# Kernel tuning notes

Hardware: AMD Instinct MI355X
Metric: run time of the kernel (lower is better)

Reference implementation:

```python
import jax, jax.numpy as jnp
import numpy as np

WINDOW = (2, 7, 7)
SHIFT = (1, 3, 3)
HEADS = 4


def _rel_pos_index(ws):
    coords = np.stack(np.meshgrid(*[np.arange(w) for w in ws], indexing='ij'))  # (3, wd, wh, ww)
    cf = coords.reshape(3, -1)
    rel = cf[:, :, None] - cf[:, None, :]  # (3, N, N)
    rel = rel.transpose(1, 2, 0).astype(np.int64)
    rel[:, :, 0] += ws[0] - 1
    rel[:, :, 1] += ws[1] - 1
    rel[:, :, 2] += ws[2] - 1
    rel[:, :, 0] *= (2 * ws[1] - 1) * (2 * ws[2] - 1)
    rel[:, :, 1] *= 2 * ws[2] - 1
    return rel.sum(-1)  # (N, N)


def _attn_mask(D, H, W, ws, ss):
    img = np.zeros((1, D, H, W, 1), np.float32)
    cnt = 0
    for d in (slice(None, -ws[0]), slice(-ws[0], -ss[0]), slice(-ss[0], None)):
        for h in (slice(None, -ws[1]), slice(-ws[1], -ss[1]), slice(-ss[1], None)):
            for w in (slice(None, -ws[2]), slice(-ws[2], -ss[2]), slice(-ss[2], None)):
                img[:, d, h, w, :] = cnt
                cnt += 1
    N = ws[0] * ws[1] * ws[2]
    mw = img.reshape(1, D // ws[0], ws[0], H // ws[1], ws[1], W // ws[2], ws[2], 1)
    mw = mw.transpose(0, 1, 3, 5, 2, 4, 6, 7).reshape(-1, N)  # (nW, N)
    diff = mw[:, None, :] - mw[:, :, None]
    return np.where(diff != 0, -100.0, 0.0).astype(np.float32)  # (nW, N, N)


def _win_partition(x, ws):
    B, D, H, W, C = x.shape
    x = x.reshape(B, D // ws[0], ws[0], H // ws[1], ws[1], W // ws[2], ws[2], C)
    return x.transpose(0, 1, 3, 5, 2, 4, 6, 7).reshape(-1, ws[0] * ws[1] * ws[2], C)


def _win_reverse(win, ws, B, D, H, W):
    C = win.shape[-1]
    x = win.reshape(B, D // ws[0], H // ws[1], W // ws[2], ws[0], ws[1], ws[2], C)
    return x.transpose(0, 1, 4, 2, 5, 3, 6, 7).reshape(B, D, H, W, C)


def _ln(x, w, b):
    mu = x.mean(-1, keepdims=True)
    var = x.var(-1, keepdims=True)
    return (x - mu) / jnp.sqrt(var + 1e-5) * w + b


def setup_inputs() -> dict:
    key = jax.random.key(0)
    ks = jax.random.split(key, 8)
    B, D, H, W, C = 4, 8, 56, 56, 128
    hidden = 4 * C
    table = (2 * WINDOW[0] - 1) * (2 * WINDOW[1] - 1) * (2 * WINDOW[2] - 1)
    return {
        'x': jax.random.normal(ks[0], (B, D, H, W, C), jnp.float32),
        'norm1_w': jnp.ones((C,), jnp.float32),
        'norm1_b': jnp.zeros((C,), jnp.float32),
        'qkv_w': 0.02 * jax.random.normal(ks[1], (3 * C, C), jnp.float32),
        'qkv_b': jnp.zeros((3 * C,), jnp.float32),
        'rpb': 0.02 * jax.random.normal(ks[2], (table, HEADS), jnp.float32),
        'proj_w': 0.02 * jax.random.normal(ks[3], (C, C), jnp.float32),
        'proj_b': jnp.zeros((C,), jnp.float32),
        'norm2_w': jnp.ones((C,), jnp.float32),
        'norm2_b': jnp.zeros((C,), jnp.float32),
        'fc1_w': 0.02 * jax.random.normal(ks[4], (hidden, C), jnp.float32),
        'fc1_b': jnp.zeros((hidden,), jnp.float32),
        'fc2_w': 0.02 * jax.random.normal(ks[5], (C, hidden), jnp.float32),
        'fc2_b': jnp.zeros((C,), jnp.float32),
    }


def reference(x, norm1_w, norm1_b, qkv_w, qkv_b, rpb, proj_w, proj_b,
              norm2_w, norm2_b, fc1_w, fc1_b, fc2_w, fc2_b):
    B, D, H, W, C = x.shape
    hd = C // HEADS
    scale = hd ** -0.5
    N = WINDOW[0] * WINDOW[1] * WINDOW[2]

    shortcut = x
    y = _ln(x, norm1_w, norm1_b)
    # cyclic shift (SW-MSA)
    y = jnp.roll(y, (-SHIFT[0], -SHIFT[1], -SHIFT[2]), axis=(1, 2, 3))
    win = _win_partition(y, WINDOW)  # (B_, N, C)
    B_ = win.shape[0]

    qkv = win @ qkv_w.T + qkv_b  # (B_, N, 3C)
    qkv = qkv.reshape(B_, N, 3, HEADS, hd).transpose(2, 0, 3, 1, 4)
    q, k, v = qkv[0] * scale, qkv[1], qkv[2]  # (B_, h, N, hd)

    attn = jnp.einsum('bhnd,bhmd->bhnm', q, k)  # (B_, h, N, N)
    rpi = _rel_pos_index(WINDOW)
    bias = rpb[rpi.reshape(-1)].reshape(N, N, HEADS).transpose(2, 0, 1)  # (h, N, N)
    attn = attn + bias[None]

    mask = jnp.asarray(_attn_mask(D, H, W, WINDOW, SHIFT))  # (nW, N, N)
    nW = mask.shape[0]
    attn = attn.reshape(B_ // nW, nW, HEADS, N, N) + mask[None, :, None]
    attn = jax.nn.softmax(attn.reshape(B_, HEADS, N, N), axis=-1)

    out = jnp.einsum('bhnm,bhmd->bhnd', attn, v)
    out = out.transpose(0, 2, 1, 3).reshape(B_, N, C)
    out = out @ proj_w.T + proj_b

    y = _win_reverse(out, WINDOW, B, D, H, W)
    y = jnp.roll(y, SHIFT, axis=(1, 2, 3))  # reverse cyclic shift
    x = shortcut + y

    h = _ln(x, norm2_w, norm2_b)
    h = jax.nn.gelu(h @ fc1_w.T + fc1_b, approximate=False)
    h = h @ fc2_w.T + fc2_b
    return x + h
```

## Files before the change

### kernel.cpp

```cpp
#include <hip/hip_runtime.h>
#include <math.h>

typedef short bf16x8 __attribute__((ext_vector_type(8)));
typedef float f32x4 __attribute__((ext_vector_type(4)));
typedef unsigned short u16;

#define DEVFN static __device__ __forceinline__

DEVFN u16 f2bf(float f) {
  union { float f; unsigned u; } v; v.f = f;
  return (u16)((v.u + 0x7FFFu + ((v.u >> 16) & 1u)) >> 16);
}

DEVFN void gload16(const void* g, void* l) {
  __builtin_amdgcn_global_load_lds(
      (const __attribute__((address_space(1))) void*)g,
      (__attribute__((address_space(3))) void*)l, 16, 0, 0);
}

DEVFN float gelu_fast(float x) {
  float e = __expf(-1.702f * x);
  return x * __builtin_amdgcn_rcpf(1.0f + e);
}

#define TT 100352
#define BWIN 1024

__global__ void convert4_kernel(const float* __restrict__ a, const float* __restrict__ b,
                                const float* __restrict__ c, const float* __restrict__ d,
                                u16* __restrict__ oa, u16* __restrict__ ob,
                                u16* __restrict__ oc, u16* __restrict__ od) {
  int i = blockIdx.x * 256 + threadIdx.x;
  const float* s; u16* o; int off;
  if (i < 49152)       { s = a; o = oa; off = i; }
  else if (i < 65536)  { s = b; o = ob; off = i - 49152; }
  else if (i < 131072) { s = c; o = oc; off = i - 65536; }
  else                 { s = d; o = od; off = i - 131072; }
  o[off] = f2bf(s[off]);
}

__global__ void bias_kernel(const float* __restrict__ rpb, float* __restrict__ bias_full) {
  int idx = blockIdx.x * 256 + threadIdx.x;
  if (idx >= 4 * 9604) return;
  int h = idx / 9604, rem = idx % 9604, i = rem / 98, j = rem % 98;
  int di = i / 49, ri = i % 49, hi = ri / 7, wi = ri % 7;
  int dj = j / 49, rj = j % 49, hj = rj / 7, wj = rj % 7;
  int tidx = (di - dj + 1) * 169 + (hi - hj + 6) * 13 + (wi - wj + 6);
  bias_full[idx] = rpb[tidx * 4 + h];
}

__global__ __launch_bounds__(256) void ln_kernel(const float* __restrict__ x,
    const float* __restrict__ w, const float* __restrict__ bterm, u16* __restrict__ out)
{
  int gw = blockIdx.x * 4 + (threadIdx.x >> 6);
  int lane = threadIdx.x & 63;
  int b_ = gw / 98, n = gw % 98;
  int bb = b_ >> 8, widx = b_ & 255;
  int dw = widx >> 6, hw = (widx >> 3) & 7, ww = widx & 7;
  int dd = n / 49, rr = n % 49, hh = rr / 7, wn = rr % 7;
  int d = (dw * 2 + dd + 1) & 7;
  int h = hw * 7 + hh + 3; if (h >= 56) h -= 56;
  int wq = ww * 7 + wn + 3; if (wq >= 56) wq -= 56;
  size_t src = ((size_t)(((bb * 8 + d) * 56 + h) * 56 + wq)) * 128;
  float2 v = *(const float2*)(x + src + lane * 2);
  float s = v.x + v.y, q = v.x * v.x + v.y * v.y;
  #pragma unroll
  for (int m = 1; m < 64; m <<= 1) { s += __shfl_xor(s, m, 64); q += __shfl_xor(q, m, 64); }
  float mu = s * (1.0f / 128.0f);
  float var = q * (1.0f / 128.0f) - mu * mu;
  float rstd = rsqrtf(var + 1e-5f);
  int c = lane * 2;
  float y0 = (v.x - mu) * rstd * w[c] + bterm[c];
  float y1 = (v.y - mu) * rstd * w[c + 1] + bterm[c + 1];
  ushort2 o; o.x = f2bf(y0); o.y = f2bf(y1);
  *(ushort2*)(out + (size_t)gw * 128 + c) = o;
}

template<int EPI>
__global__ __launch_bounds__(256) void gemm_kernel(
    const u16* __restrict__ A, const u16* __restrict__ Bw,
    const float* __restrict__ bias, const float* __restrict__ res,
    void* __restrict__ outp, const float* __restrict__ n2w,
    const float* __restrict__ n2b, u16* __restrict__ h1out,
    int M, int N, int K)
{
  __shared__ u16 smem[EPI == 1 ? 17664 : 16384];
  u16* As = smem;
  u16* Bs = smem + 8192;
  const int m0 = blockIdx.x * 128, n0 = blockIdx.y * 128;
  const int t = threadIdx.x;
  const int wid = t >> 6, lane = t & 63;
  const int wr = wid >> 1, wc = wid & 1;
  const int l15 = lane & 15, lhi = lane >> 4;
  const int srow = lane >> 3;
  const int sslot = lane & 7;
  const int gcol = ((sslot ^ srow) << 3);
  f32x4 acc[4][4] = {};
  for (int k0 = 0; k0 < K; k0 += 64) {
    #pragma unroll
    for (int it = 0; it < 4; ++it) {
      const int rbase = it * 32 + wid * 8;
      const int row = rbase + srow;
      gload16(A + (size_t)(m0 + row) * K + k0 + gcol, As + rbase * 64);
      gload16(Bw + (size_t)(n0 + row) * K + k0 + gcol, Bs + rbase * 64);
    }
    __syncthreads();
    #pragma unroll
    for (int kk = 0; kk < 64; kk += 32) {
      bf16x8 af[4], bfr[4];
      const int csw = (kk + lhi * 8) ^ ((l15 & 7) << 3);
      #pragma unroll
      for (int mi = 0; mi < 4; ++mi) af[mi] = *(const bf16x8*)(As + (wr * 64 + mi * 16 + l15) * 64 + csw);
      #pragma unroll
      for (int ni = 0; ni < 4; ++ni) bfr[ni] = *(const bf16x8*)(Bs + (wc * 64 + ni * 16 + l15) * 64 + csw);
      #pragma unroll
      for (int mi = 0; mi < 4; ++mi)
        #pragma unroll
        for (int ni = 0; ni < 4; ++ni)
          acc[mi][ni] = __builtin_amdgcn_mfma_f32_16x16x32_bf16(af[mi], bfr[ni], acc[mi][ni], 0, 0, 0);
    }
    __syncthreads();
  }
  if (EPI == 0) {
    const float smul = (n0 == 0) ? 0.17677669529663689f : 1.0f;
    #pragma unroll
    for (int mi = 0; mi < 4; ++mi)
      #pragma unroll
      for (int ni = 0; ni < 4; ++ni) {
        int col = wc * 64 + ni * 16 + l15;
        float bcol = bias[n0 + col];
        #pragma unroll
        for (int r = 0; r < 4; ++r) {
          int row = wr * 64 + mi * 16 + lhi * 4 + r;
          float v = (acc[mi][ni][r] + bcol) * smul;
          smem[row * 128 + (((col >> 3) ^ (row & 7)) << 3) + (col & 7)] = f2bf(v);
        }
      }
    __syncthreads();
    const int rsub = t >> 4, sl = t & 15;
    #pragma unroll
    for (int j = 0; j < 8; ++j) {
      int row = j * 16 + rsub;
      int4 val = *(const int4*)(smem + row * 128 + ((sl ^ (row & 7)) << 3));
      *(int4*)((u16*)outp + (size_t)(m0 + row) * N + n0 + sl * 8) = val;
    }
  } else {
    float* Pk = (float*)smem;
    #pragma unroll
    for (int half = 0; half < 2; ++half) {
      if (wr == half) {
        #pragma unroll
        for (int ni = 0; ni < 4; ++ni) {
          int col = wc * 64 + ni * 16 + l15;
          float bcol = bias[col];
          #pragma unroll
          for (int mi = 0; mi < 4; ++mi)
            #pragma unroll
            for (int r = 0; r < 4; ++r)
              Pk[(mi * 16 + lhi * 4 + r) * 138 + col] = acc[mi][ni][r] + bcol;
        }
      }
      __syncthreads();
      {
        int rowl = t >> 2, q = t & 3;
        int grow = m0 + half * 64 + rowl;
        int b_ = grow / 98, n = grow % 98;
        int bb = b_ >> 8, widx = b_ & 255;
        int dw = widx >> 6, hw = (widx >> 3) & 7, ww = widx & 7;
        int dd = n / 49, rr = n % 49, hh = rr / 7, wn = rr % 7;
        int d = (dw * 2 + dd + 1) & 7;
        int hq = hw * 7 + hh + 3; if (hq >= 56) hq -= 56;
        int wq = ww * 7 + wn + 3; if (wq >= 56) wq -= 56;
        size_t dbase = ((size_t)(((bb * 8 + d) * 56 + hq) * 56 + wq)) * 128;
        f32x4 vals[8];
        float s = 0.f, sq = 0.f;
        #pragma unroll
        for (int j = 0; j < 8; ++j) {
          int col = j * 16 + q * 4;
          f32x4 pv = *(const f32x4*)(Pk + rowl * 138 + col);
          f32x4 rv = *(const f32x4*)(res + dbase + col);
          f32x4 v = pv + rv;
          vals[j] = v;
          *(f32x4*)((float*)outp + dbase + col) = v;
          s += v[0] + v[1] + v[2] + v[3];
          sq += v[0]*v[0] + v[1]*v[1] + v[2]*v[2] + v[3]*v[3];
        }
        s += __shfl_xor(s, 1, 64);  sq += __shfl_xor(sq, 1, 64);
        s += __shfl_xor(s, 2, 64);  sq += __shfl_xor(sq, 2, 64);
        float mu = s * (1.0f / 128.0f);
        float var = sq * (1.0f / 128.0f) - mu * mu;
        float rstd = rsqrtf(var + 1e-5f);
        #pragma unroll
        for (int j = 0; j < 8; ++j) {
          int col = j * 16 + q * 4;
          f32x4 wv = *(const f32x4*)(n2w + col);
          f32x4 bv = *(const f32x4*)(n2b + col);
          u16 hb[4];
          #pragma unroll
          for (int e = 0; e < 4; ++e)
            hb[e] = f2bf((vals[j][e] - mu) * rstd * wv[e] + bv[e]);
          *(int2*)(h1out + dbase + col) = *(const int2*)hb;
        }
      }
      __syncthreads();
    }
  }
}

__global__ __launch_bounds__(256, 2) void mlp_kernel(
    const u16* __restrict__ A, const u16* __restrict__ W1, const float* __restrict__ b1,
    const u16* __restrict__ W2, const float* __restrict__ b2,
    const float* __restrict__ res, float* __restrict__ outp)
{
  __shared__ u16 smem[34816];
  u16* W1c = smem;
  u16* W2c = smem + 8192;
  u16* HsA = smem + 24576;
  float* b1s = (float*)(smem + 33792);
  float* Pk = (float*)smem;
  const int m0 = blockIdx.x * 128;
  const int t = threadIdx.x, wid = t >> 6, lane = t & 63;
  const int l15 = lane & 15, lhi = lane >> 4;
  const int srow4 = lane >> 4, sslot16 = lane & 15;
  const int srow8 = lane >> 3, sslot8 = lane & 7;
  u16* hs = HsA + wid * 2304;

  #pragma unroll
  for (int it = 0; it < 4; ++it) {
    int rb1 = it * 16 + wid * 4, r1 = rb1 + srow4;
    gload16(W1 + (size_t)r1 * 128 + ((sslot16 ^ (r1 & 7)) << 3), W1c + rb1 * 128);
    int rb2 = it * 32 + wid * 8, r2 = rb2 + srow8;
    gload16(W2 + (size_t)r2 * 512 + ((sslot8 ^ (r2 & 7)) << 3), W2c + rb2 * 64);
  }
  if (t < 128) *(f32x4*)(b1s + t * 4) = *(const f32x4*)(b1 + t * 4);
  bf16x8 areg[2][4];
  #pragma unroll
  for (int mi = 0; mi < 2; ++mi)
    #pragma unroll
    for (int kg = 0; kg < 4; ++kg)
      areg[mi][kg] = *(const bf16x8*)(A + (size_t)(m0 + wid * 32 + mi * 16 + l15) * 128 + kg * 32 + lhi * 8);

  f32x4 accO[2][8] = {};
  __syncthreads();
  for (int hc = 0; hc < 8; ++hc) {
    const int cur = (hc & 1) * 8192;
    if (hc < 7) {
      const int nxt = ((hc + 1) & 1) * 8192;
      #pragma unroll
      for (int it = 0; it < 4; ++it) {
        int rb2 = it * 32 + wid * 8, r2 = rb2 + srow8;
        gload16(W2 + (size_t)r2 * 512 + (hc + 1) * 64 + ((sslot8 ^ (r2 & 7)) << 3),
                W2c + nxt + rb2 * 64);
      }
    }
    f32x4 accH[2][4] = {};
    #pragma unroll
    for (int kk = 0; kk < 4; ++kk) {
      bf16x8 bw[4];
      #pragma unroll
      for (int ni = 0; ni < 4; ++ni) {
        int row = ni * 16 + l15;
        bw[ni] = *(const bf16x8*)(W1c + row * 128 + (((kk * 4 + lhi) ^ (row & 7)) << 3));
      }
      #pragma unroll
      for (int mi = 0; mi < 2; ++mi)
        #pragma unroll
        for (int ni = 0; ni < 4; ++ni)
          accH[mi][ni] = __builtin_amdgcn_mfma_f32_16x16x32_bf16(areg[mi][kk], bw[ni], accH[mi][ni], 0, 0, 0);
    }
    #pragma unroll
    for (int mi = 0; mi < 2; ++mi)
      #pragma unroll
      for (int ni = 0; ni < 4; ++ni) {
        float bb = b1s[hc * 64 + ni * 16 + l15];
        #pragma unroll
        for (int r = 0; r < 4; ++r) {
          int tokl = mi * 16 + lhi * 4 + r;
          hs[tokl * 72 + ni * 16 + l15] = f2bf(gelu_fast(accH[mi][ni][r] + bb));
        }
      }
    __syncthreads();
    if (hc < 7) {
      #pragma unroll
      for (int it = 0; it < 4; ++it) {
        int rb1 = it * 16 + wid * 4, r1 = rb1 + srow4;
        gload16(W1 + (size_t)((hc + 1) * 64 + r1) * 128 + ((sslot16 ^ (r1 & 7)) << 3),
                W1c + rb1 * 128);
      }
    }
    #pragma unroll
    for (int kk = 0; kk < 2; ++kk) {
      bf16x8 ah[2], bw2[8];
      #pragma unroll
      for (int mi = 0; mi < 2; ++mi)
        ah[mi] = *(const bf16x8*)(hs + (mi * 16 + l15) * 72 + kk * 32 + lhi * 8);
      #pragma unroll
      for (int ni = 0; ni < 8; ++ni) {
        int row = ni * 16 + l15;
        bw2[ni] = *(const bf16x8*)(W2c + cur + row * 64 + (((kk * 4 + lhi) ^ (row & 7)) << 3));
      }
      #pragma unroll
      for (int mi = 0; mi < 2; ++mi)
        #pragma unroll
        for (int ni = 0; ni < 8; ++ni)
          accO[mi][ni] = __builtin_amdgcn_mfma_f32_16x16x32_bf16(ah[mi], bw2[ni], accO[mi][ni], 0, 0, 0);
    }
    __syncthreads();
  }
  #pragma unroll
  for (int half = 0; half < 2; ++half) {
    if ((wid >> 1) == half) {
      #pragma unroll
      for (int ni = 0; ni < 8; ++ni) {
        int col = ni * 16 + l15;
        float bv = b2[col];
        #pragma unroll
        for (int mi = 0; mi < 2; ++mi)
          #pragma unroll
          for (int r = 0; r < 4; ++r) {
            int tokl = (wid & 1) * 32 + mi * 16 + lhi * 4 + r;
            Pk[tokl * 132 + col] = accO[mi][ni][r] + bv;
          }
      }
    }
    __syncthreads();
    #pragma unroll
    for (int p = 0; p < 8; ++p) {
      int idx = p * 256 + t;
      int row = idx >> 5, c = (idx & 31) * 4;
      size_t gtok = (size_t)(m0 + half * 64 + row);
      f32x4 v = *(const f32x4*)(Pk + row * 132 + c);
      f32x4 rv = *(const f32x4*)(res + gtok * 128 + c);
      *(f32x4*)(outp + gtok * 128 + c) = v + rv;
    }
    __syncthreads();
  }
}

__global__ __launch_bounds__(64) void attn_kernel(
    const u16* __restrict__ qkv, const float* __restrict__ bias_full,
    u16* __restrict__ out_win)
{
  __shared__ u16 k_lds[112][40];
  __shared__ u16 vT[32][136];
  __shared__ u16 P[16][136];
  __shared__ signed char rids[112];
  const int bid = blockIdx.x;
  const int w = bid >> 2, h = bid & 3;
  const int lane = threadIdx.x;
  const int l15 = lane & 15, lhi = lane >> 4;
  const int widx = w & 255;
  const int dw = widx >> 6, hw = (widx >> 3) & 7, ww = widx & 7;

  #pragma unroll
  for (int rep = 0; rep < 2; ++rep) {
    int t2 = lane + rep * 64;
    if (t2 < 112) {
      int rv = 0;
      if (t2 < 98) {
        int dd = t2 / 49, rr = t2 % 49, hh = rr / 7, wn = rr % 7;
        int dp = dw * 2 + dd, hp = hw * 7 + hh, wp = ww * 7 + wn;
        int rd = dp < 6 ? 0 : (dp < 7 ? 1 : 2);
        int rh = hp < 49 ? 0 : (hp < 53 ? 1 : 2);
        int rw2 = wp < 49 ? 0 : (wp < 53 ? 1 : 2);
        rv = rd * 9 + rh * 3 + rw2;
      }
      rids[t2] = (signed char)rv;
    }
  }
  for (int f = lane; f < 160; f += 64) {
    int d = f / 5, c = 96 + (f % 5) * 8;
    *(int4*)&vT[d][c] = (int4){0, 0, 0, 0};
  }
  if (lane < 48) {
    int r = lane / 3, c = 112 + (lane % 3) * 8;
    *(int4*)&P[r][c] = (int4){0, 0, 0, 0};
  }
  const size_t base = (size_t)w * 98 * 384;
  for (int f = lane; f < 448; f += 64) {
    int n = f >> 2, c = (f & 3) * 8;
    int4 v = (int4){0, 0, 0, 0};
    if (n < 98) v = *(const int4*)(qkv + base + (size_t)n * 384 + 128 + h * 32 + c);
    *(int4*)(&k_lds[n][c]) = v;
  }
  for (int f = lane; f < 392; f += 64) {
    int n = f >> 2, c = (f & 3) * 8;
    int4 v = *(const int4*)(qkv + base + (size_t)n * 384 + 256 + h * 32 + c);
    const u16* pv = (const u16*)&v;
    #pragma unroll
    for (int j = 0; j < 8; ++j) vT[c + j][n] = pv[j];
  }
  __syncthreads();

  const float* bh = bias_full + h * 9604;
  const size_t obase = (size_t)w * 98 * 128;
  for (int mt = 0; mt < 7; ++mt) {
    int qn = mt * 16 + l15; if (qn > 97) qn = 97;
    bf16x8 aq = *(const bf16x8*)(qkv + base + (size_t)qn * 384 + h * 32 + lhi * 8);
    f32x4 sf[7];
    #pragma unroll
    for (int nt = 0; nt < 7; ++nt) {
      bf16x8 bk = *(const bf16x8*)(&k_lds[nt * 16 + l15][lhi * 8]);
      f32x4 z = {0.f, 0.f, 0.f, 0.f};
      sf[nt] = __builtin_amdgcn_mfma_f32_16x16x32_bf16(aq, bk, z, 0, 0, 0);
    }
    int irow[4], ridr[4];
    #pragma unroll
    for (int r = 0; r < 4; ++r) {
      irow[r] = mt * 16 + lhi * 4 + r;
      ridr[r] = rids[irow[r] > 111 ? 111 : irow[r]];
    }
    float mx[4] = {-1e30f, -1e30f, -1e30f, -1e30f};
    #pragma unroll
    for (int nt = 0; nt < 7; ++nt) {
      int j = nt * 16 + l15;
      int jc = j > 97 ? 97 : j;
      int rj = rids[j];
      #pragma unroll
      for (int r = 0; r < 4; ++r) {
        float s = sf[nt][r];
        int ic = irow[r] > 97 ? 97 : irow[r];
        s += bh[ic * 98 + jc];
        if (ridr[r] != rj) s -= 100.0f;
        if (j > 97) s = -1e30f;
        sf[nt][r] = s;
        mx[r] = fmaxf(mx[r], s);
      }
    }
    #pragma unroll
    for (int m = 1; m < 16; m <<= 1)
      #pragma unroll
      for (int r = 0; r < 4; ++r) mx[r] = fmaxf(mx[r], __shfl_xor(mx[r], m, 64));
    float sm[4] = {0.f, 0.f, 0.f, 0.f};
    #pragma unroll
    for (int nt = 0; nt < 7; ++nt)
      #pragma unroll
      for (int r = 0; r < 4; ++r) {
        float p = __expf(sf[nt][r] - mx[r]);
        sf[nt][r] = p;
        sm[r] += p;
      }
    #pragma unroll
    for (int m = 1; m < 16; m <<= 1)
      #pragma unroll
      for (int r = 0; r < 4; ++r) sm[r] += __shfl_xor(sm[r], m, 64);
    float inv[4];
    #pragma unroll
    for (int r = 0; r < 4; ++r) inv[r] = 1.0f / sm[r];
    __syncthreads();
    #pragma unroll
    for (int nt = 0; nt < 7; ++nt)
      #pragma unroll
      for (int r = 0; r < 4; ++r)
        P[lhi * 4 + r][nt * 16 + l15] = f2bf(sf[nt][r] * inv[r]);
    __syncthreads();
    f32x4 o0 = {}, o1 = {};
    #pragma unroll
    for (int ks = 0; ks < 4; ++ks) {
      bf16x8 ap  = *(const bf16x8*)(&P[l15][ks * 32 + lhi * 8]);
      bf16x8 bv0 = *(const bf16x8*)(&vT[l15][ks * 32 + lhi * 8]);
      bf16x8 bv1 = *(const bf16x8*)(&vT[16 + l15][ks * 32 + lhi * 8]);
      o0 = __builtin_amdgcn_mfma_f32_16x16x32_bf16(ap, bv0, o0, 0, 0, 0);
      o1 = __builtin_amdgcn_mfma_f32_16x16x32_bf16(ap, bv1, o1, 0, 0, 0);
    }
    #pragma unroll
    for (int r = 0; r < 4; ++r) {
      if (irow[r] < 98) {
        size_t orow = obase + (size_t)irow[r] * 128 + h * 32;
        out_win[orow + l15] = f2bf(o0[r]);
        out_win[orow + 16 + l15] = f2bf(o1[r]);
      }
    }
  }
}

extern "C" void kernel_launch(void* const* d_in, const int* in_sizes, int n_in,
                              void* d_out, int out_size, void* d_ws, size_t ws_size,
                              hipStream_t stream)
{
  const float* x      = (const float*)d_in[0];
  const float* n1w    = (const float*)d_in[1];
  const float* n1b    = (const float*)d_in[2];
  const float* qkv_w  = (const float*)d_in[3];
  const float* qkv_b  = (const float*)d_in[4];
  const float* rpb    = (const float*)d_in[5];
  const float* proj_w = (const float*)d_in[6];
  const float* proj_b = (const float*)d_in[7];
  const float* n2w    = (const float*)d_in[8];
  const float* n2b    = (const float*)d_in[9];
  const float* fc1_w  = (const float*)d_in[10];
  const float* fc1_b  = (const float*)d_in[11];
  const float* fc2_w  = (const float*)d_in[12];
  const float* fc2_b  = (const float*)d_in[13];

  char* p = (char*)d_ws;
  size_t off = 0;
  auto alloc = [&](size_t bytes) { void* r = p + off; off = (off + bytes + 255) & ~(size_t)255; return r; };
  u16*   qkvw_b    = (u16*)alloc(49152 * 2);
  u16*   projw_b   = (u16*)alloc(16384 * 2);
  u16*   fc1w_b    = (u16*)alloc(65536 * 2);
  u16*   fc2w_b    = (u16*)alloc(65536 * 2);
  float* bias_full = (float*)alloc(4 * 9604 * 4);
  u16*   y_win     = (u16*)alloc((size_t)TT * 128 * 2);
  float* x2        = (float*)alloc((size_t)TT * 128 * 4);
  u16*   h1        = (u16*)alloc((size_t)TT * 128 * 2);
  u16*   big       = (u16*)alloc((size_t)TT * 384 * 2);
  if (off > ws_size) return;

  convert4_kernel<<<768, 256, 0, stream>>>(qkv_w, proj_w, fc1_w, fc2_w,
                                           qkvw_b, projw_b, fc1w_b, fc2w_b);
  bias_kernel<<<(4 * 9604 + 255) / 256, 256, 0, stream>>>(rpb, bias_full);
  ln_kernel<<<TT / 4, 256, 0, stream>>>(x, n1w, n1b, y_win);
  gemm_kernel<0><<<dim3(TT / 128, 3), 256, 0, stream>>>(y_win, qkvw_b, qkv_b, nullptr, big,
                                                        nullptr, nullptr, nullptr, TT, 384, 128);
  attn_kernel<<<BWIN * 4, 64, 0, stream>>>(big, bias_full, y_win);
  gemm_kernel<1><<<dim3(TT / 128, 1), 256, 0, stream>>>(y_win, projw_b, proj_b, x, x2,
                                                        n2w, n2b, h1, TT, 128, 128);
  mlp_kernel<<<TT / 128, 256, 0, stream>>>(h1, fc1w_b, fc1_b, fc2w_b, fc2_b, x2, (float*)d_out);
}
```

Measured before the change: 226.5 us.

## Precompute fused bias+mask in MFMA fragment layout; load K directly from global

Replaces the per-head bias table and the per-block region-id mask with a table that merges relative-position bias and shift mask. The table is laid out in MFMA accumulator fragment order for each of the 8 window boundary patterns, so each lane reads it with one coalesced float4 load. K fragments are now read straight from global memory instead of being staged in LDS. The barriers are dropped, which relies on each block being a single wavefront. This removes scattered bias gathers, integer mask logic and LDS staging, at the cost of a larger precomputed table and repeated global K reads.

```diff
diff --git a/kernel.cpp b/kernel.cpp
--- a/kernel.cpp
+++ b/kernel.cpp
@@ -39,14 +39,37 @@
   o[off] = f2bf(s[off]);
 }
 
-__global__ void bias_kernel(const float* __restrict__ rpb, float* __restrict__ bias_full) {
+__global__ void biasmask_kernel(const float* __restrict__ rpb, float* __restrict__ bm) {
   int idx = blockIdx.x * 256 + threadIdx.x;
-  if (idx >= 4 * 9604) return;
-  int h = idx / 9604, rem = idx % 9604, i = rem / 98, j = rem % 98;
-  int di = i / 49, ri = i % 49, hi = ri / 7, wi = ri % 7;
-  int dj = j / 49, rj = j % 49, hj = rj / 7, wj = rj % 7;
-  int tidx = (di - dj + 1) * 169 + (hi - hj + 6) * 13 + (wi - wj + 6);
-  bias_full[idx] = rpb[tidx * 4 + h];
+  int lane = idx & 63;
+  int rem = idx >> 6;
+  int nt = rem % 7;  rem /= 7;
+  int mt = rem % 7;  rem /= 7;
+  int h = rem & 3;
+  int pat = rem >> 2;
+  int dB = (pat >> 2) & 1, hB = (pat >> 1) & 1, wB = pat & 1;
+  int jc = nt * 16 + (lane & 15);
+  f32x4 out;
+  #pragma unroll
+  for (int r = 0; r < 4; ++r) {
+    int ic = mt * 16 + (lane >> 4) * 4 + r;
+    float v;
+    if (jc > 97) v = -30000.f;
+    else if (ic > 97) v = 0.f;
+    else {
+      int di = ic / 49, ri = ic % 49, hi = ri / 7, wi = ri % 7;
+      int dj = jc / 49, rj = jc % 49, hj = rj / 7, wj = rj % 7;
+      int tidx = (di - dj + 1) * 169 + (hi - hj + 6) * 13 + (wi - wj + 6);
+      v = rpb[tidx * 4 + h];
+      int ridi = (dB ? (di == 0 ? 1 : 2) * 9 : 0) + (hB ? (hi < 4 ? 1 : 2) * 3 : 0)
+               + (wB ? (wi < 4 ? 1 : 2) : 0);
+      int ridj = (dB ? (dj == 0 ? 1 : 2) * 9 : 0) + (hB ? (hj < 4 ? 1 : 2) * 3 : 0)
+               + (wB ? (wj < 4 ? 1 : 2) : 0);
+      if (ridi != ridj) v -= 100.f;
+    }
+    out[r] = v;
+  }
+  *(f32x4*)(bm + (size_t)idx * 4) = out;
 }
 
 __global__ __launch_bounds__(256) void ln_kernel(const float* __restrict__ x,
@@ -338,36 +361,20 @@
 }
 
 __global__ __launch_bounds__(64) void attn_kernel(
-    const u16* __restrict__ qkv, const float* __restrict__ bias_full,
+    const u16* __restrict__ qkv, const float* __restrict__ biasmask,
     u16* __restrict__ out_win)
 {
-  __shared__ u16 k_lds[112][40];
   __shared__ u16 vT[32][136];
   __shared__ u16 P[16][136];
-  __shared__ signed char rids[112];
   const int bid = blockIdx.x;
   const int w = bid >> 2, h = bid & 3;
   const int lane = threadIdx.x;
   const int l15 = lane & 15, lhi = lane >> 4;
   const int widx = w & 255;
   const int dw = widx >> 6, hw = (widx >> 3) & 7, ww = widx & 7;
-
-  #pragma unroll
-  for (int rep = 0; rep < 2; ++rep) {
-    int t2 = lane + rep * 64;
-    if (t2 < 112) {
-      int rv = 0;
-      if (t2 < 98) {
-        int dd = t2 / 49, rr = t2 % 49, hh = rr / 7, wn = rr % 7;
-        int dp = dw * 2 + dd, hp = hw * 7 + hh, wp = ww * 7 + wn;
-        int rd = dp < 6 ? 0 : (dp < 7 ? 1 : 2);
-        int rh = hp < 49 ? 0 : (hp < 53 ? 1 : 2);
-        int rw2 = wp < 49 ? 0 : (wp < 53 ? 1 : 2);
-        rv = rd * 9 + rh * 3 + rw2;
-      }
-      rids[t2] = (signed char)rv;
-    }
-  }
+  const int pat = ((dw == 3) ? 4 : 0) | ((hw == 7) ? 2 : 0) | ((ww == 7) ? 1 : 0);
+  const float* bmh = biasmask + (size_t)(pat * 4 + h) * (49 * 256);
+
   for (int f = lane; f < 160; f += 64) {
     int d = f / 5, c = 96 + (f % 5) * 8;
     *(int4*)&vT[d][c] = (int4){0, 0, 0, 0};
@@ -377,12 +384,6 @@
     *(int4*)&P[r][c] = (int4){0, 0, 0, 0};
   }
   const size_t base = (size_t)w * 98 * 384;
-  for (int f = lane; f < 448; f += 64) {
-    int n = f >> 2, c = (f & 3) * 8;
-    int4 v = (int4){0, 0, 0, 0};
-    if (n < 98) v = *(const int4*)(qkv + base + (size_t)n * 384 + 128 + h * 32 + c);
-    *(int4*)(&k_lds[n][c]) = v;
-  }
   for (int f = lane; f < 392; f += 64) {
     int n = f >> 2, c = (f & 3) * 8;
     int4 v = *(const int4*)(qkv + base + (size_t)n * 384 + 256 + h * 32 + c);
@@ -390,9 +391,6 @@
     #pragma unroll
     for (int j = 0; j < 8; ++j) vT[c + j][n] = pv[j];
   }
-  __syncthreads();
-
-  const float* bh = bias_full + h * 9604;
   const size_t obase = (size_t)w * 98 * 128;
   for (int mt = 0; mt < 7; ++mt) {
     int qn = mt * 16 + l15; if (qn > 97) qn = 97;
@@ -400,29 +398,18 @@
     f32x4 sf[7];
     #pragma unroll
     for (int nt = 0; nt < 7; ++nt) {
-      bf16x8 bk = *(const bf16x8*)(&k_lds[nt * 16 + l15][lhi * 8]);
+      int kn = nt * 16 + l15; if (kn > 97) kn = 97;
+      bf16x8 bk = *(const bf16x8*)(qkv + base + (size_t)kn * 384 + 128 + h * 32 + lhi * 8);
       f32x4 z = {0.f, 0.f, 0.f, 0.f};
       sf[nt] = __builtin_amdgcn_mfma_f32_16x16x32_bf16(aq, bk, z, 0, 0, 0);
     }
-    int irow[4], ridr[4];
-    #pragma unroll
-    for (int r = 0; r < 4; ++r) {
-      irow[r] = mt * 16 + lhi * 4 + r;
-      ridr[r] = rids[irow[r] > 111 ? 111 : irow[r]];
-    }
     float mx[4] = {-1e30f, -1e30f, -1e30f, -1e30f};
     #pragma unroll
     for (int nt = 0; nt < 7; ++nt) {
-      int j = nt * 16 + l15;
-      int jc = j > 97 ? 97 : j;
-      int rj = rids[j];
+      f32x4 bm = *(const f32x4*)(bmh + (mt * 7 + nt) * 256 + lane * 4);
       #pragma unroll
       for (int r = 0; r < 4; ++r) {
-        float s = sf[nt][r];
-        int ic = irow[r] > 97 ? 97 : irow[r];
-        s += bh[ic * 98 + jc];
-        if (ridr[r] != rj) s -= 100.0f;
-        if (j > 97) s = -1e30f;
+        float s = sf[nt][r] + bm[r];
         sf[nt][r] = s;
         mx[r] = fmaxf(mx[r], s);
       }
@@ -447,13 +434,11 @@
     float inv[4];
     #pragma unroll
     for (int r = 0; r < 4; ++r) inv[r] = 1.0f / sm[r];
-    __syncthreads();
     #pragma unroll
     for (int nt = 0; nt < 7; ++nt)
       #pragma unroll
       for (int r = 0; r < 4; ++r)
         P[lhi * 4 + r][nt * 16 + l15] = f2bf(sf[nt][r] * inv[r]);
-    __syncthreads();
     f32x4 o0 = {}, o1 = {};
     #pragma unroll
     for (int ks = 0; ks < 4; ++ks) {
@@ -463,10 +448,11 @@
       o0 = __builtin_amdgcn_mfma_f32_16x16x32_bf16(ap, bv0, o0, 0, 0, 0);
       o1 = __builtin_amdgcn_mfma_f32_16x16x32_bf16(ap, bv1, o1, 0, 0, 0);
     }
+    int irow0 = mt * 16 + lhi * 4;
     #pragma unroll
     for (int r = 0; r < 4; ++r) {
-      if (irow[r] < 98) {
-        size_t orow = obase + (size_t)irow[r] * 128 + h * 32;
+      if (irow0 + r < 98) {
+        size_t orow = obase + (size_t)(irow0 + r) * 128 + h * 32;
         out_win[orow + l15] = f2bf(o0[r]);
         out_win[orow + 16 + l15] = f2bf(o1[r]);
       }
@@ -500,7 +486,7 @@
   u16*   projw_b   = (u16*)alloc(16384 * 2);
   u16*   fc1w_b    = (u16*)alloc(65536 * 2);
   u16*   fc2w_b    = (u16*)alloc(65536 * 2);
-  float* bias_full = (float*)alloc(4 * 9604 * 4);
+  float* biasmask  = (float*)alloc(8 * 4 * 49 * 256 * 4);
   u16*   y_win     = (u16*)alloc((size_t)TT * 128 * 2);
   float* x2        = (float*)alloc((size_t)TT * 128 * 4);
   u16*   h1        = (u16*)alloc((size_t)TT * 128 * 2);
@@ -509,11 +495,11 @@
 
   convert4_kernel<<<768, 256, 0, stream>>>(qkv_w, proj_w, fc1_w, fc2_w,
                                            qkvw_b, projw_b, fc1w_b, fc2w_b);
-  bias_kernel<<<(4 * 9604 + 255) / 256, 256, 0, stream>>>(rpb, bias_full);
+  biasmask_kernel<<<392, 256, 0, stream>>>(rpb, biasmask);
   ln_kernel<<<TT / 4, 256, 0, stream>>>(x, n1w, n1b, y_win);
   gemm_kernel<0><<<dim3(TT / 128, 3), 256, 0, stream>>>(y_win, qkvw_b, qkv_b, nullptr, big,
                                                         nullptr, nullptr, nullptr, TT, 384, 128);
-  attn_kernel<<<BWIN * 4, 64, 0, stream>>>(big, bias_full, y_win);
+  attn_kernel<<<BWIN * 4, 64, 0, stream>>>(big, biasmask, y_win);
   gemm_kernel<1><<<dim3(TT / 128, 1), 256, 0, stream>>>(y_win, projw_b, proj_b, x, x2,
                                                         n2w, n2b, h1, TT, 128, 128);
   mlp_kernel<<<TT / 128, 256, 0, stream>>>(h1, fc1w_b, fc1_b, fc2w_b, fc2_b, x2, (float*)d_out);
```

New measurement: 199.7 us. 11.8% less time.
